# Kernel tuning notes

Measured on AMD Instinct MI355X. Metric: run time of the kernel, lower is better.

Reference implementation:

```python
import jax, jax.numpy as jnp
import numpy as np

H = 512
W = 512
N = 2048          # number of gaussians
B = 65536         # pixel batch
MU_BORDER = 1.05
S_MIN = 1.0 / 30.0    # 1 / n_gaussian_max_pixels
S_MAX = 1.0 / 0.75    # 1 / n_gaussian_min_pixels
PI_APPROX = 3.1416    # module uses 3.1416, not math.pi


def setup_inputs() -> dict:
    key = jax.random.key(0)
    k0, k1, k2, k3, k4 = jax.random.split(key, 5)
    # pixel coordinates in [0,W]x[0,H]
    x = jax.random.uniform(k0, (B, 2), dtype=jnp.float32) * jnp.array([W, H], jnp.float32)
    rgb = jax.random.normal(k1, (N, 3), dtype=jnp.float32)
    mu = jax.random.uniform(k2, (N, 2), dtype=jnp.float32) * 2.0 - 1.0
    scale = jax.random.normal(k3, (N, 2), dtype=jnp.float32) * 0.5
    angle = jax.random.normal(k4, (N,), dtype=jnp.float32) * 0.5
    return {"x": x, "rgb": rgb, "mu": mu, "scale": scale, "angle": angle}


def reference(x, rgb, mu, scale, angle):
    wh = jnp.array([W, H], jnp.float32)                    # [2]
    xn = x / wh * 2.0 - 1.0                                # [B,2] in [-1,1]
    mu_t = jnp.tanh(mu) * MU_BORDER                        # [N,2]
    # (x - mu) / 2 * wh  -> pairwise offset in pixel units
    vec = (xn[:, None, :] - mu_t[None, :, :]) * 0.5 * wh   # [B,N,2]
    alpha = jnp.tanh(angle) * PI_APPROX                    # [N]
    c = jnp.cos(alpha)                                     # [N]
    s = jnp.sin(alpha)                                     # [N]
    S = jax.nn.sigmoid(scale) * (S_MAX - S_MIN) + S_MIN    # [N,2]
    vx, vy = vec[..., 0], vec[..., 1]                      # [B,N] each
    # d1 = diag(S) @ R(alpha) @ vec ; R = [[c,-s],[s,c]]
    d1x = S[:, 0] * (c * vx - s * vy)                      # [B,N]
    d1y = S[:, 1] * (s * vx + c * vy)                      # [B,N]
    w_bn = jnp.exp(-(d1x * d1x + d1y * d1y))               # [B,N]
    rgb_n3 = jax.nn.sigmoid(rgb)                           # [N,3]
    return jnp.einsum('bn,nc->bc', w_bn, rgb_n3)           # [B,3]
```

## Files before the change

### kernel.cpp

```cpp
#include <hip/hip_runtime.h>

#define NGAUSS 2048
#define NPIX   65536
#define WID    512.0f
#define HEI    512.0f

#define NTX     8
#define NTY     8
#define NTILE   (NTX * NTY)
#define TSHIFT  6
#define GCAP    2048
#define PCAP    2048
#define TPB     256
#define NCHUNK  (PCAP / TPB)
#define PREP_NB (NGAUSS / TPB)
#define BIN_NB  32
#define BIN_PPB (NPIX / BIN_NB)
#define BIN_PPT (BIN_PPB / TPB)

#define SQRT_CUT 5.2f

#define WS_PRM_OFF   0
#define WS_GCNT_OFF  98304
#define WS_PCNT_OFF  98560
#define WS_GLIST_OFF 98816
#define WS_PLIST_OFF (98816 + 524288)
#define WS_NEED      (WS_PLIST_OFF + 524288)


__global__ __launch_bounds__(256) void setup_kernel(
    const float2* __restrict__ x, const float* __restrict__ rgb,
    const float* __restrict__ mu, const float* __restrict__ scale,
    const float* __restrict__ angle, float4* __restrict__ prm,
    unsigned* __restrict__ gcount, unsigned* __restrict__ glist,
    unsigned* __restrict__ pcount, unsigned* __restrict__ plist)
{
    __shared__ unsigned lcnt[NTILE];
    __shared__ unsigned lbase[NTILE];

    const int tid = threadIdx.x;
    if (tid < NTILE) lcnt[tid] = 0u;

    if (blockIdx.x < PREP_NB) {
        const int n = blockIdx.x * TPB + tid;

        const float MU_BORDER = 1.05f;
        const float S_MIN = 1.0f / 30.0f;
        const float S_MAX = 1.0f / 0.75f;
        const float PI_APPROX = 3.1416f;
        const float K = 1.2011224087864498f;

        float mx = tanhf(mu[2*n+0]) * MU_BORDER * (0.5f * WID);
        float my = tanhf(mu[2*n+1]) * MU_BORDER * (0.5f * HEI);
        float al = tanhf(angle[n]) * PI_APPROX;
        float c = cosf(al);
        float s = sinf(al);
        float S0 = 1.0f / (1.0f + expf(-scale[2*n+0])) * (S_MAX - S_MIN) + S_MIN;
        float S1 = 1.0f / (1.0f + expf(-scale[2*n+1])) * (S_MAX - S_MIN) + S_MIN;

        float A  =  S0 * c * K;
        float Bc = -(S0 * s * K);
        float C  =  S1 * s * K;
        float D  =  S1 * c * K;
        float E0 = -(A * mx + Bc * my);
        float E1 = -(C * mx + D  * my);

        float r = 1.0f / (1.0f + expf(-rgb[3*n+0]));
        float g = 1.0f / (1.0f + expf(-rgb[3*n+1]));
        float b = 1.0f / (1.0f + expf(-rgb[3*n+2]));

        prm[3*n + 0] = make_float4(A, Bc, C, D);
        prm[3*n + 1] = make_float4(E0, E1, r, g);
        prm[3*n + 2] = make_float4(b, 0.f, 0.f, 0.f);

        float i0 = 1.0f / S0, i1 = 1.0f / S1;
        float hx = (SQRT_CUT / K) * sqrtf(c*c*i0*i0 + s*s*i1*i1);
        float hy = (SQRT_CUT / K) * sqrtf(s*s*i0*i0 + c*c*i1*i1);
        float px = mx + 0.5f * WID;
        float py = my + 0.5f * HEI;

        int ix0 = (int)floorf(px - hx), ix1 = (int)floorf(px + hx);
        int iy0 = (int)floorf(py - hy), iy1 = (int)floorf(py + hy);
        int tx0 = max(0, ix0 >> TSHIFT), tx1 = min(NTX - 1, ix1 >> TSHIFT);
        int ty0 = max(0, iy0 >> TSHIFT), ty1 = min(NTY - 1, iy1 >> TSHIFT);

        __syncthreads();
        for (int ty = ty0; ty <= ty1; ++ty)
            for (int tx = tx0; tx <= tx1; ++tx)
                atomicAdd(&lcnt[ty * NTX + tx], 1u);
        __syncthreads();
        if (tid < NTILE) {
            lbase[tid] = atomicAdd(&gcount[tid], lcnt[tid]);
            lcnt[tid] = 0u;
        }
        __syncthreads();
        for (int ty = ty0; ty <= ty1; ++ty)
            for (int tx = tx0; tx <= tx1; ++tx) {
                int t = ty * NTX + tx;
                unsigned slot = lbase[t] + atomicAdd(&lcnt[t], 1u);
                if (slot < GCAP) glist[t * GCAP + slot] = (unsigned)n;
            }
    } else {
        const int start = (blockIdx.x - PREP_NB) * BIN_PPB;
        __syncthreads();

        unsigned tcache[BIN_PPT];
        #pragma unroll
        for (int k = 0; k < BIN_PPT; ++k) {
            int b = start + k * TPB + tid;
            float2 p = x[b];
            int tx = min(NTX - 1, max(0, ((int)p.x) >> TSHIFT));
            int ty = min(NTY - 1, max(0, ((int)p.y) >> TSHIFT));
            unsigned t = (unsigned)(ty * NTX + tx);
            tcache[k] = t;
            atomicAdd(&lcnt[t], 1u);
        }
        __syncthreads();
        if (tid < NTILE) {
            lbase[tid] = atomicAdd(&pcount[tid], lcnt[tid]);
            lcnt[tid] = 0u;
        }
        __syncthreads();
        #pragma unroll
        for (int k = 0; k < BIN_PPT; ++k) {
            int b = start + k * TPB + tid;
            unsigned t = tcache[k];
            unsigned slot = lbase[t] + atomicAdd(&lcnt[t], 1u);
            if (slot < PCAP) plist[t * PCAP + slot] = (unsigned)b;
        }
    }
}

__global__ __launch_bounds__(256) void splat_tile(
    const float2* __restrict__ x, const float4* __restrict__ prm,
    const unsigned* __restrict__ gcount, const unsigned* __restrict__ glist,
    const unsigned* __restrict__ pcount, const unsigned* __restrict__ plist,
    float* __restrict__ out)
{
    __shared__ float4 sg[TPB * 3];

    const int t     = blockIdx.x;
    const int tid   = threadIdx.x;
    const unsigned pcnt = min(pcount[t], (unsigned)PCAP);
    const unsigned base = blockIdx.y * TPB;
    if (base >= pcnt) return;

    const bool valid = (base + tid) < pcnt;
    unsigned slot = base + (valid ? (unsigned)tid : 0u);
    unsigned pid  = plist[t * PCAP + slot];
    float2 p = x[pid];
    float X = p.x - 0.5f * WID;
    float Y = p.y - 0.5f * HEI;

    const unsigned gcnt = min(gcount[t], (unsigned)GCAP);
    float ar = 0.f, ag = 0.f, ab = 0.f;

    for (unsigned g0 = 0; g0 < gcnt; g0 += TPB) {
        __syncthreads();
        unsigned gi = g0 + tid;
        if (gi < gcnt) {
            unsigned n = glist[t * GCAP + gi];
            sg[3*tid + 0] = prm[3*n + 0];
            sg[3*tid + 1] = prm[3*n + 1];
            sg[3*tid + 2] = prm[3*n + 2];
        }
        __syncthreads();

        unsigned cnt = min((unsigned)TPB, gcnt - g0);
        #pragma unroll 4
        for (unsigned j = 0; j < cnt; ++j) {
            float4 c0 = sg[3*j + 0];
            float4 c1 = sg[3*j + 1];
            float4 c2 = sg[3*j + 2];
            float dx = fmaf(c0.x, X, fmaf(c0.y, Y, c1.x));
            float dy = fmaf(c0.z, X, fmaf(c0.w, Y, c1.y));
            float q  = fmaf(dx, dx, dy * dy);
            float w  = __builtin_amdgcn_exp2f(-q);
            ar = fmaf(w, c1.z, ar);
            ag = fmaf(w, c1.w, ag);
            ab = fmaf(w, c2.x, ab);
        }
    }

    if (valid) {
        out[3*pid + 0] = ar;
        out[3*pid + 1] = ag;
        out[3*pid + 2] = ab;
    }
}

#define NSLICE 16
#define GPB    (NGAUSS / NSLICE)
#define PPB    512

__global__ __launch_bounds__(256) void splat_flat(
    const float2* __restrict__ x, const float* __restrict__ rgb,
    const float* __restrict__ mu, const float* __restrict__ scale,
    const float* __restrict__ angle, float* __restrict__ out)
{
    __shared__ float4 sh4[GPB * 2];
    __shared__ float  shb[GPB];

    const int slice = blockIdx.x & (NSLICE - 1);
    const int pg    = blockIdx.x >> 4;
    const int tid   = threadIdx.x;

    if (tid < GPB) {
        const float MU_BORDER = 1.05f;
        const float S_MIN = 1.0f / 30.0f;
        const float S_MAX = 1.0f / 0.75f;
        const float PI_APPROX = 3.1416f;
        const float K = 1.2011224087864498f;

        int n = slice * GPB + tid;
        float mx = tanhf(mu[2*n+0]) * MU_BORDER * (0.5f * WID);
        float my = tanhf(mu[2*n+1]) * MU_BORDER * (0.5f * HEI);
        float al = tanhf(angle[n]) * PI_APPROX;
        float c = cosf(al);
        float s = sinf(al);
        float S0 = 1.0f / (1.0f + expf(-scale[2*n+0])) * (S_MAX - S_MIN) + S_MIN;
        float S1 = 1.0f / (1.0f + expf(-scale[2*n+1])) * (S_MAX - S_MIN) + S_MIN;
        float A  =  S0 * c * K;
        float Bc = -(S0 * s * K);
        float C  =  S1 * s * K;
        float D  =  S1 * c * K;
        sh4[2*tid + 0] = make_float4(A, Bc, C, D);
        sh4[2*tid + 1] = make_float4(-(A * mx + Bc * my), -(C * mx + D * my),
                                     1.0f / (1.0f + expf(-rgb[3*n+0])),
                                     1.0f / (1.0f + expf(-rgb[3*n+1])));
        shb[tid] = 1.0f / (1.0f + expf(-rgb[3*n+2]));
    }
    __syncthreads();

    const int t0 = pg * PPB + tid;
    const int t1 = t0 + TPB;
    float2 xy0 = x[t0];
    float2 xy1 = x[t1];
    float X0 = xy0.x - 0.5f * WID, Y0 = xy0.y - 0.5f * HEI;
    float X1 = xy1.x - 0.5f * WID, Y1 = xy1.y - 0.5f * HEI;

    float ar0 = 0.f, ag0 = 0.f, ab0 = 0.f;
    float ar1 = 0.f, ag1 = 0.f, ab1 = 0.f;
    #pragma unroll 4
    for (int j = 0; j < GPB; ++j) {
        float4 c0 = sh4[2*j + 0];
        float4 c1 = sh4[2*j + 1];
        float bb  = shb[j];
        float dx0 = fmaf(c0.x, X0, fmaf(c0.y, Y0, c1.x));
        float dy0 = fmaf(c0.z, X0, fmaf(c0.w, Y0, c1.y));
        float w0  = __builtin_amdgcn_exp2f(-fmaf(dx0, dx0, dy0 * dy0));
        float dx1 = fmaf(c0.x, X1, fmaf(c0.y, Y1, c1.x));
        float dy1 = fmaf(c0.z, X1, fmaf(c0.w, Y1, c1.y));
        float w1  = __builtin_amdgcn_exp2f(-fmaf(dx1, dx1, dy1 * dy1));
        ar0 = fmaf(w0, c1.z, ar0); ag0 = fmaf(w0, c1.w, ag0); ab0 = fmaf(w0, bb, ab0);
        ar1 = fmaf(w1, c1.z, ar1); ag1 = fmaf(w1, c1.w, ag1); ab1 = fmaf(w1, bb, ab1);
    }

    atomicAdd(&out[3*t0 + 0], ar0);
    atomicAdd(&out[3*t0 + 1], ag0);
    atomicAdd(&out[3*t0 + 2], ab0);
    atomicAdd(&out[3*t1 + 0], ar1);
    atomicAdd(&out[3*t1 + 1], ag1);
    atomicAdd(&out[3*t1 + 2], ab1);
}

extern "C" void kernel_launch(void* const* d_in, const int* in_sizes, int n_in,
                              void* d_out, int out_size, void* d_ws, size_t ws_size,
                              hipStream_t stream) {
    const float* x     = (const float*)d_in[0];
    const float* rgb   = (const float*)d_in[1];
    const float* mu    = (const float*)d_in[2];
    const float* scale = (const float*)d_in[3];
    const float* angle = (const float*)d_in[4];

    if (ws_size >= (size_t)WS_NEED && d_ws != nullptr) {
        char* ws = (char*)d_ws;
        float4*   prm    = (float4*)(ws + WS_PRM_OFF);
        unsigned* gcount = (unsigned*)(ws + WS_GCNT_OFF);
        unsigned* pcount = (unsigned*)(ws + WS_PCNT_OFF);
        unsigned* glist  = (unsigned*)(ws + WS_GLIST_OFF);
        unsigned* plist  = (unsigned*)(ws + WS_PLIST_OFF);

        hipMemsetAsync(ws + WS_GCNT_OFF, 0, 512, stream);

        hipLaunchKernelGGL(setup_kernel, dim3(PREP_NB + BIN_NB), dim3(TPB), 0, stream,
                           (const float2*)x, rgb, mu, scale, angle,
                           prm, gcount, glist, pcount, plist);
        hipLaunchKernelGGL(splat_tile, dim3(NTILE, NCHUNK), dim3(TPB), 0, stream,
                           (const float2*)x, prm, gcount, glist, pcount, plist,
                           (float*)d_out);
    } else {
        hipMemsetAsync(d_out, 0, (size_t)out_size * sizeof(float), stream);
        hipLaunchKernelGGL(splat_flat, dim3(NPIX / PPB * NSLICE), dim3(TPB), 0, stream,
                           (const float2*)x, rgb, mu, scale, angle, (float*)d_out);
    }
}
```

Measured before the change: 75.69 us.

## Fuse setup and splat into one cooperative kernel with per-block segmented lists

After: 183.5 us. +142.4%, slower.

```diff
diff --git a/kernel.cpp b/kernel.cpp
--- a/kernel.cpp
+++ b/kernel.cpp
@@ -1,4 +1,7 @@
 #include <hip/hip_runtime.h>
+#include <hip/hip_cooperative_groups.h>
+
+namespace cg = cooperative_groups;
 
 #define NGAUSS 2048
 #define NPIX   65536
@@ -9,157 +12,168 @@
 #define NTY     8
 #define NTILE   (NTX * NTY)
 #define TSHIFT  6
-#define GCAP    2048
-#define PCAP    2048
 #define TPB     256
-#define NCHUNK  (PCAP / TPB)
+
 #define PREP_NB (NGAUSS / TPB)
+#define GSEG    TPB
+#define GT      (PREP_NB * GSEG)
+
 #define BIN_NB  32
 #define BIN_PPB (NPIX / BIN_NB)
 #define BIN_PPT (BIN_PPB / TPB)
+#define PSEG    BIN_PPB
+#define PT      (BIN_NB * PSEG)
+
+#define NCHUNK  8
+#define SPLAT_NB (NTILE * NCHUNK)
 
 #define SQRT_CUT 5.2f
 
 #define WS_PRM_OFF   0
-#define WS_GCNT_OFF  98304
-#define WS_PCNT_OFF  98560
-#define WS_GLIST_OFF 98816
-#define WS_PLIST_OFF (98816 + 524288)
-#define WS_NEED      (WS_PLIST_OFF + 524288)
-
-
-__global__ __launch_bounds__(256) void setup_kernel(
-    const float2* __restrict__ x, const float* __restrict__ rgb,
-    const float* __restrict__ mu, const float* __restrict__ scale,
-    const float* __restrict__ angle, float4* __restrict__ prm,
-    unsigned* __restrict__ gcount, unsigned* __restrict__ glist,
-    unsigned* __restrict__ pcount, unsigned* __restrict__ plist)
-{
-    __shared__ unsigned lcnt[NTILE];
-    __shared__ unsigned lbase[NTILE];
-
+#define WS_GSEG_OFF  98304
+#define WS_PSEG_OFF  (WS_GSEG_OFF + NTILE*PREP_NB*4)
+#define WS_GLIST_OFF (WS_PSEG_OFF + NTILE*BIN_NB*4)
+#define WS_PLIST_OFF (WS_GLIST_OFF + NTILE*GT*4)
+#define WS_NEED      (WS_PLIST_OFF + NTILE*PT*4)
+
+
+__device__ __forceinline__ void do_bin(
+    int bb, const float2* __restrict__ x,
+    unsigned* __restrict__ pseg_cnt, unsigned* __restrict__ plist,
+    unsigned* lcnt )
+{
     const int tid = threadIdx.x;
     if (tid < NTILE) lcnt[tid] = 0u;
-
-    if (blockIdx.x < PREP_NB) {
-        const int n = blockIdx.x * TPB + tid;
-
-        const float MU_BORDER = 1.05f;
-        const float S_MIN = 1.0f / 30.0f;
-        const float S_MAX = 1.0f / 0.75f;
-        const float PI_APPROX = 3.1416f;
-        const float K = 1.2011224087864498f;
-
-        float mx = tanhf(mu[2*n+0]) * MU_BORDER * (0.5f * WID);
-        float my = tanhf(mu[2*n+1]) * MU_BORDER * (0.5f * HEI);
-        float al = tanhf(angle[n]) * PI_APPROX;
-        float c = cosf(al);
-        float s = sinf(al);
-        float S0 = 1.0f / (1.0f + expf(-scale[2*n+0])) * (S_MAX - S_MIN) + S_MIN;
-        float S1 = 1.0f / (1.0f + expf(-scale[2*n+1])) * (S_MAX - S_MIN) + S_MIN;
-
-        float A  =  S0 * c * K;
-        float Bc = -(S0 * s * K);
-        float C  =  S1 * s * K;
-        float D  =  S1 * c * K;
-        float E0 = -(A * mx + Bc * my);
-        float E1 = -(C * mx + D  * my);
-
-        float r = 1.0f / (1.0f + expf(-rgb[3*n+0]));
-        float g = 1.0f / (1.0f + expf(-rgb[3*n+1]));
-        float b = 1.0f / (1.0f + expf(-rgb[3*n+2]));
-
-        prm[3*n + 0] = make_float4(A, Bc, C, D);
-        prm[3*n + 1] = make_float4(E0, E1, r, g);
-        prm[3*n + 2] = make_float4(b, 0.f, 0.f, 0.f);
-
-        float i0 = 1.0f / S0, i1 = 1.0f / S1;
-        float hx = (SQRT_CUT / K) * sqrtf(c*c*i0*i0 + s*s*i1*i1);
-        float hy = (SQRT_CUT / K) * sqrtf(s*s*i0*i0 + c*c*i1*i1);
-        float px = mx + 0.5f * WID;
-        float py = my + 0.5f * HEI;
-
-        int ix0 = (int)floorf(px - hx), ix1 = (int)floorf(px + hx);
-        int iy0 = (int)floorf(py - hy), iy1 = (int)floorf(py + hy);
-        int tx0 = max(0, ix0 >> TSHIFT), tx1 = min(NTX - 1, ix1 >> TSHIFT);
-        int ty0 = max(0, iy0 >> TSHIFT), ty1 = min(NTY - 1, iy1 >> TSHIFT);
-
-        __syncthreads();
-        for (int ty = ty0; ty <= ty1; ++ty)
-            for (int tx = tx0; tx <= tx1; ++tx)
-                atomicAdd(&lcnt[ty * NTX + tx], 1u);
-        __syncthreads();
-        if (tid < NTILE) {
-            lbase[tid] = atomicAdd(&gcount[tid], lcnt[tid]);
-            lcnt[tid] = 0u;
+    __syncthreads();
+
+    const int start = bb * BIN_PPB;
+    #pragma unroll
+    for (int k = 0; k < BIN_PPT; ++k) {
+        int b = start + k * TPB + tid;
+        float2 p = x[b];
+        int tx = min(NTX - 1, max(0, ((int)p.x) >> TSHIFT));
+        int ty = min(NTY - 1, max(0, ((int)p.y) >> TSHIFT));
+        unsigned t = (unsigned)(ty * NTX + tx);
+        unsigned slot = atomicAdd(&lcnt[t], 1u);
+        plist[t * PT + bb * PSEG + slot] = (unsigned)b;
+    }
+    __syncthreads();
+    if (tid < NTILE) pseg_cnt[tid * BIN_NB + bb] = lcnt[tid];
+}
+
+__device__ __forceinline__ void do_prep(
+    int pb, const float* __restrict__ rgb, const float* __restrict__ mu,
+    const float* __restrict__ scale, const float* __restrict__ angle,
+    float4* __restrict__ prm, unsigned* __restrict__ gseg_cnt,
+    unsigned* __restrict__ glist, unsigned* lcnt )
+{
+    const int tid = threadIdx.x;
+    if (tid < NTILE) lcnt[tid] = 0u;
+
+    const int n = pb * TPB + tid;
+
+    const float MU_BORDER = 1.05f;
+    const float S_MIN = 1.0f / 30.0f;
+    const float S_MAX = 1.0f / 0.75f;
+    const float PI_APPROX = 3.1416f;
+    const float K = 1.2011224087864498f;
+
+    float mx = tanhf(mu[2*n+0]) * MU_BORDER * (0.5f * WID);
+    float my = tanhf(mu[2*n+1]) * MU_BORDER * (0.5f * HEI);
+    float al = tanhf(angle[n]) * PI_APPROX;
+    float c = cosf(al);
+    float s = sinf(al);
+    float S0 = 1.0f / (1.0f + expf(-scale[2*n+0])) * (S_MAX - S_MIN) + S_MIN;
+    float S1 = 1.0f / (1.0f + expf(-scale[2*n+1])) * (S_MAX - S_MIN) + S_MIN;
+
+    float A  =  S0 * c * K;
+    float Bc = -(S0 * s * K);
+    float C  =  S1 * s * K;
+    float D  =  S1 * c * K;
+    float E0 = -(A * mx + Bc * my);
+    float E1 = -(C * mx + D  * my);
+
+    float r = 1.0f / (1.0f + expf(-rgb[3*n+0]));
+    float g = 1.0f / (1.0f + expf(-rgb[3*n+1]));
+    float b = 1.0f / (1.0f + expf(-rgb[3*n+2]));
+
+    prm[3*n + 0] = make_float4(A, Bc, C, D);
+    prm[3*n + 1] = make_float4(E0, E1, r, g);
+    prm[3*n + 2] = make_float4(b, 0.f, 0.f, 0.f);
+
+    float i0 = 1.0f / S0, i1 = 1.0f / S1;
+    float hx = (SQRT_CUT / K) * sqrtf(c*c*i0*i0 + s*s*i1*i1);
+    float hy = (SQRT_CUT / K) * sqrtf(s*s*i0*i0 + c*c*i1*i1);
+    float px = mx + 0.5f * WID;
+    float py = my + 0.5f * HEI;
+
+    int ix0 = (int)floorf(px - hx), ix1 = (int)floorf(px + hx);
+    int iy0 = (int)floorf(py - hy), iy1 = (int)floorf(py + hy);
+    int tx0 = max(0, ix0 >> TSHIFT), tx1 = min(NTX - 1, ix1 >> TSHIFT);
+    int ty0 = max(0, iy0 >> TSHIFT), ty1 = min(NTY - 1, iy1 >> TSHIFT);
+
+    __syncthreads();
+    for (int ty = ty0; ty <= ty1; ++ty)
+        for (int tx = tx0; tx <= tx1; ++tx) {
+            int t = ty * NTX + tx;
+            unsigned slot = atomicAdd(&lcnt[t], 1u);
+            glist[t * GT + pb * GSEG + slot] = (unsigned)n;
         }
-        __syncthreads();
-        for (int ty = ty0; ty <= ty1; ++ty)
-            for (int tx = tx0; tx <= tx1; ++tx) {
-                int t = ty * NTX + tx;
-                unsigned slot = lbase[t] + atomicAdd(&lcnt[t], 1u);
-                if (slot < GCAP) glist[t * GCAP + slot] = (unsigned)n;
-            }
-    } else {
-        const int start = (blockIdx.x - PREP_NB) * BIN_PPB;
-        __syncthreads();
-
-        unsigned tcache[BIN_PPT];
+    __syncthreads();
+    if (tid < NTILE) gseg_cnt[tid * PREP_NB + pb] = lcnt[tid];
+}
+
+__device__ __forceinline__ void do_splat(
+    int t, int chunk, const float2* __restrict__ x,
+    const float4* __restrict__ prm,
+    const unsigned* __restrict__ gseg_cnt, const unsigned* __restrict__ pseg_cnt,
+    const unsigned* __restrict__ glist, const unsigned* __restrict__ plist,
+    float* __restrict__ out,
+    float4* sg , unsigned* prefP ,
+    unsigned* prefG )
+{
+    const int tid = threadIdx.x;
+
+    if (tid == 0) {
+        unsigned acc = 0;
+        prefP[0] = 0;
         #pragma unroll
-        for (int k = 0; k < BIN_PPT; ++k) {
-            int b = start + k * TPB + tid;
-            float2 p = x[b];
-            int tx = min(NTX - 1, max(0, ((int)p.x) >> TSHIFT));
-            int ty = min(NTY - 1, max(0, ((int)p.y) >> TSHIFT));
-            unsigned t = (unsigned)(ty * NTX + tx);
-            tcache[k] = t;
-            atomicAdd(&lcnt[t], 1u);
-        }
-        __syncthreads();
-        if (tid < NTILE) {
-            lbase[tid] = atomicAdd(&pcount[tid], lcnt[tid]);
-            lcnt[tid] = 0u;
-        }
-        __syncthreads();
+        for (int i = 0; i < BIN_NB; ++i) { acc += pseg_cnt[t * BIN_NB + i]; prefP[i+1] = acc; }
+        acc = 0;
+        prefG[0] = 0;
         #pragma unroll
-        for (int k = 0; k < BIN_PPT; ++k) {
-            int b = start + k * TPB + tid;
-            unsigned t = tcache[k];
-            unsigned slot = lbase[t] + atomicAdd(&lcnt[t], 1u);
-            if (slot < PCAP) plist[t * PCAP + slot] = (unsigned)b;
-        }
-    }
-}
-
-__global__ __launch_bounds__(256) void splat_tile(
-    const float2* __restrict__ x, const float4* __restrict__ prm,
-    const unsigned* __restrict__ gcount, const unsigned* __restrict__ glist,
-    const unsigned* __restrict__ pcount, const unsigned* __restrict__ plist,
-    float* __restrict__ out)
-{
-    __shared__ float4 sg[TPB * 3];
-
-    const int t     = blockIdx.x;
-    const int tid   = threadIdx.x;
-    const unsigned pcnt = min(pcount[t], (unsigned)PCAP);
-    const unsigned base = blockIdx.y * TPB;
-    if (base >= pcnt) return;
-
-    const bool valid = (base + tid) < pcnt;
-    unsigned slot = base + (valid ? (unsigned)tid : 0u);
-    unsigned pid  = plist[t * PCAP + slot];
+        for (int i = 0; i < PREP_NB; ++i) { acc += gseg_cnt[t * PREP_NB + i]; prefG[i+1] = acc; }
+    }
+    __syncthreads();
+
+    const unsigned pcnt = min(prefP[BIN_NB], (unsigned)(NCHUNK * TPB));
+    const unsigned gidx = (unsigned)(chunk * TPB + tid);
+    if ((unsigned)(chunk * TPB) >= pcnt) return;
+
+    const bool valid = gidx < pcnt;
+    unsigned gq = valid ? gidx : 0u;
+    int s = 0;
+    #pragma unroll
+    for (int step = 16; step >= 1; step >>= 1)
+        if (prefP[s + step] <= gq) s += step;
+    unsigned pid = plist[t * PT + s * PSEG + (gq - prefP[s])];
+
     float2 p = x[pid];
     float X = p.x - 0.5f * WID;
     float Y = p.y - 0.5f * HEI;
 
-    const unsigned gcnt = min(gcount[t], (unsigned)GCAP);
+    const unsigned gcnt = prefG[PREP_NB];
     float ar = 0.f, ag = 0.f, ab = 0.f;
 
     for (unsigned g0 = 0; g0 < gcnt; g0 += TPB) {
         __syncthreads();
         unsigned gi = g0 + tid;
         if (gi < gcnt) {
-            unsigned n = glist[t * GCAP + gi];
+            int gs = 0;
+            #pragma unroll
+            for (int step = 4; step >= 1; step >>= 1)
+                if (prefG[gs + step] <= gi) gs += step;
+            unsigned n = glist[t * GT + gs * GSEG + (gi - prefG[gs])];
             sg[3*tid + 0] = prm[3*n + 0];
             sg[3*tid + 1] = prm[3*n + 1];
             sg[3*tid + 2] = prm[3*n + 2];
@@ -187,6 +201,59 @@
         out[3*pid + 1] = ag;
         out[3*pid + 2] = ab;
     }
+}
+
+__global__ __launch_bounds__(256) void fused_kernel(
+    const float2* __restrict__ x, const float* __restrict__ rgb,
+    const float* __restrict__ mu, const float* __restrict__ scale,
+    const float* __restrict__ angle, float4* __restrict__ prm,
+    unsigned* __restrict__ gseg_cnt, unsigned* __restrict__ pseg_cnt,
+    unsigned* __restrict__ glist, unsigned* __restrict__ plist,
+    float* __restrict__ out)
+{
+    __shared__ unsigned lcnt[NTILE];
+    __shared__ float4   sg[TPB * 3];
+    __shared__ unsigned prefP[BIN_NB + 1];
+    __shared__ unsigned prefG[PREP_NB + 1];
+
+    const int bid = blockIdx.x;
+    if (bid < BIN_NB) {
+        do_bin(bid, x, pseg_cnt, plist, lcnt);
+    } else if (bid < BIN_NB + PREP_NB) {
+        do_prep(bid - BIN_NB, rgb, mu, scale, angle, prm, gseg_cnt, glist, lcnt);
+    }
+    __threadfence();
+    cg::this_grid().sync();
+
+    do_splat(bid >> 3, bid & (NCHUNK - 1), x, prm, gseg_cnt, pseg_cnt,
+             glist, plist, out, sg, prefP, prefG);
+}
+
+__global__ __launch_bounds__(256) void setup_kernel(
+    const float2* __restrict__ x, const float* __restrict__ rgb,
+    const float* __restrict__ mu, const float* __restrict__ scale,
+    const float* __restrict__ angle, float4* __restrict__ prm,
+    unsigned* __restrict__ gseg_cnt, unsigned* __restrict__ pseg_cnt,
+    unsigned* __restrict__ glist, unsigned* __restrict__ plist)
+{
+    __shared__ unsigned lcnt[NTILE];
+    if (blockIdx.x < BIN_NB)
+        do_bin(blockIdx.x, x, pseg_cnt, plist, lcnt);
+    else
+        do_prep(blockIdx.x - BIN_NB, rgb, mu, scale, angle, prm, gseg_cnt, glist, lcnt);
+}
+
+__global__ __launch_bounds__(256) void splat_kernel(
+    const float2* __restrict__ x, const float4* __restrict__ prm,
+    const unsigned* __restrict__ gseg_cnt, const unsigned* __restrict__ pseg_cnt,
+    const unsigned* __restrict__ glist, const unsigned* __restrict__ plist,
+    float* __restrict__ out)
+{
+    __shared__ float4   sg[TPB * 3];
+    __shared__ unsigned prefP[BIN_NB + 1];
+    __shared__ unsigned prefG[PREP_NB + 1];
+    do_splat(blockIdx.x, blockIdx.y, x, prm, gseg_cnt, pseg_cnt,
+             glist, plist, out, sg, prefP, prefG);
 }
 
 #define NSLICE 16
@@ -267,7 +334,7 @@
 extern "C" void kernel_launch(void* const* d_in, const int* in_sizes, int n_in,
                               void* d_out, int out_size, void* d_ws, size_t ws_size,
                               hipStream_t stream) {
-    const float* x     = (const float*)d_in[0];
+    const float* xf    = (const float*)d_in[0];
     const float* rgb   = (const float*)d_in[1];
     const float* mu    = (const float*)d_in[2];
     const float* scale = (const float*)d_in[3];
@@ -275,23 +342,32 @@
 
     if (ws_size >= (size_t)WS_NEED && d_ws != nullptr) {
         char* ws = (char*)d_ws;
-        float4*   prm    = (float4*)(ws + WS_PRM_OFF);
-        unsigned* gcount = (unsigned*)(ws + WS_GCNT_OFF);
-        unsigned* pcount = (unsigned*)(ws + WS_PCNT_OFF);
-        unsigned* glist  = (unsigned*)(ws + WS_GLIST_OFF);
-        unsigned* plist  = (unsigned*)(ws + WS_PLIST_OFF);
-
-        hipMemsetAsync(ws + WS_GCNT_OFF, 0, 512, stream);
-
-        hipLaunchKernelGGL(setup_kernel, dim3(PREP_NB + BIN_NB), dim3(TPB), 0, stream,
-                           (const float2*)x, rgb, mu, scale, angle,
-                           prm, gcount, glist, pcount, plist);
-        hipLaunchKernelGGL(splat_tile, dim3(NTILE, NCHUNK), dim3(TPB), 0, stream,
-                           (const float2*)x, prm, gcount, glist, pcount, plist,
-                           (float*)d_out);
+        const float2* x2     = (const float2*)xf;
+        float4*   prm        = (float4*)(ws + WS_PRM_OFF);
+        unsigned* gseg_cnt   = (unsigned*)(ws + WS_GSEG_OFF);
+        unsigned* pseg_cnt   = (unsigned*)(ws + WS_PSEG_OFF);
+        unsigned* glist      = (unsigned*)(ws + WS_GLIST_OFF);
+        unsigned* plist      = (unsigned*)(ws + WS_PLIST_OFF);
+        float*    outp       = (float*)d_out;
+
+        void* args[] = { (void*)&x2, (void*)&rgb, (void*)&mu, (void*)&scale,
+                         (void*)&angle, (void*)&prm, (void*)&gseg_cnt,
+                         (void*)&pseg_cnt, (void*)&glist, (void*)&plist,
+                         (void*)&outp };
+        hipError_t e = hipLaunchCooperativeKernel(
+            (const void*)fused_kernel, dim3(SPLAT_NB), dim3(TPB), args, 0, stream);
+        if (e != hipSuccess) {
+            hipLaunchKernelGGL(setup_kernel, dim3(BIN_NB + PREP_NB), dim3(TPB), 0,
+                               stream, x2, rgb, mu, scale, angle,
+                               prm, gseg_cnt, pseg_cnt, glist, plist);
+            hipLaunchKernelGGL(splat_kernel, dim3(NTILE, NCHUNK), dim3(TPB), 0,
+                               stream, x2, prm, gseg_cnt, pseg_cnt, glist, plist,
+                               outp);
+        }
     } else {
         hipMemsetAsync(d_out, 0, (size_t)out_size * sizeof(float), stream);
-        hipLaunchKernelGGL(splat_flat, dim3(NPIX / PPB * NSLICE), dim3(TPB), 0, stream,
-                           (const float2*)x, rgb, mu, scale, angle, (float*)d_out);
-    }
-}
+        hipLaunchKernelGGL(splat_flat, dim3(NPIX / PPB * NSLICE), dim3(TPB), 0,
+                           stream, (const float2*)xf, rgb, mu, scale, angle,
+                           (float*)d_out);
+    }
+}
```
